# Optimization experiments

Hardware: AMD Instinct MI355X
Metric: run time of the kernel (lower is better)

Reference implementation:

```python
import jax, jax.numpy as jnp
import numpy as np

HIDDEN = 4096
N_HEADS = 32
N_KV_HEADS = 8
HEAD_DIM = HIDDEN // N_HEADS  # 128
GROUPS = N_HEADS // N_KV_HEADS  # 4
ATTN_MULT = 0.08838834764831845  # 1/sqrt(head_dim)
MAX_ATTN_VAL = 30.0
NEG_INF = -1e30


def setup_inputs() -> dict:
    key = jax.random.key(0)
    ks = jax.random.split(key, 5)
    B, S = 2, 2048
    hidden_states = jax.random.normal(ks[0], (B, S, HIDDEN), dtype=jnp.float32)
    scale = 1.0 / np.sqrt(HIDDEN)
    Wq = jax.random.normal(ks[1], (HIDDEN, N_HEADS * HEAD_DIM), dtype=jnp.float32) * scale
    Wk = jax.random.normal(ks[2], (HIDDEN, N_KV_HEADS * HEAD_DIM), dtype=jnp.float32) * scale
    Wv = jax.random.normal(ks[3], (HIDDEN, N_KV_HEADS * HEAD_DIM), dtype=jnp.float32) * scale
    Wo = jax.random.normal(ks[4], (N_HEADS * HEAD_DIM, HIDDEN), dtype=jnp.float32) * scale
    return {"hidden_states": hidden_states, "Wq": Wq, "Wk": Wk, "Wv": Wv, "Wo": Wo}


def reference(hidden_states, Wq, Wk, Wv, Wo):
    B, S, _ = hidden_states.shape
    # projections
    q = (hidden_states @ Wq).reshape(B, S, N_HEADS, HEAD_DIM).transpose(0, 2, 1, 3)      # bhsd
    k = (hidden_states @ Wk).reshape(B, S, N_KV_HEADS, HEAD_DIM).transpose(0, 2, 1, 3)   # bksd
    v = (hidden_states @ Wv).reshape(B, S, N_KV_HEADS, HEAD_DIM).transpose(0, 2, 1, 3)
    # GQA: expand kv heads to query heads
    k = jnp.repeat(k, GROUPS, axis=1)  # [B, N_HEADS, S, D]
    v = jnp.repeat(v, GROUPS, axis=1)
    # scaled scores with Grok-style tanh soft-cap
    scores = jnp.einsum('bhqd,bhkd->bhqk', q, k) * ATTN_MULT
    scores = MAX_ATTN_VAL * jnp.tanh(scores / MAX_ATTN_VAL)
    # causal mask
    causal = jnp.tril(jnp.ones((S, S), dtype=bool))
    scores = jnp.where(causal[None, None], scores, NEG_INF)
    probs = jax.nn.softmax(scores.astype(jnp.float32), axis=-1).astype(v.dtype)
    out = jnp.einsum('bhqk,bhkd->bhqd', probs, v)          # [B, H, S, D]
    out = out.transpose(0, 2, 1, 3).reshape(B, S, N_HEADS * HEAD_DIM)
    return out @ Wo
```

## Files before the change

### kernel.cpp

```cpp
#include <hip/hip_runtime.h>
#include <hip/hip_bf16.h>
#include <type_traits>
#include <cmath>

#define HIDDEN 4096
#define NHEADS 32
#define NKV 8
#define HD 128
#define BB 2
#define SS 2048
#define NTOK (BB*SS)
#define ATTN_MULT 0.08838834764831845f

using bf16x8 = __attribute__((ext_vector_type(8))) short;
using f32x4  = __attribute__((ext_vector_type(4))) float;

using gas = __attribute__((address_space(1))) const void;
using las = __attribute__((address_space(3))) void;

__device__ __forceinline__ unsigned short f2bf(float f){
  unsigned int u = __builtin_bit_cast(unsigned int, f);
  u += 0x7fffu + ((u >> 16) & 1u);
  return (unsigned short)(u >> 16);
}
__device__ __forceinline__ unsigned int cvtpk(float lo, float hi){
  unsigned int r;
  asm("v_cvt_pk_bf16_f32 %0, %1, %2" : "=v"(r) : "v"(lo), "v"(hi));
  return r;
}

__global__ void cvt_f32_bf16_k(const float* __restrict__ in, unsigned short* __restrict__ out, int n8){
  int i = blockIdx.x * blockDim.x + threadIdx.x;
  if (i >= n8) return;
  const float4* p = (const float4*)in + (size_t)i * 2;
  float4 a = p[0], b = p[1];
  bf16x8 o;
  o[0]=f2bf(a.x); o[1]=f2bf(a.y); o[2]=f2bf(a.z); o[3]=f2bf(a.w);
  o[4]=f2bf(b.x); o[5]=f2bf(b.y); o[6]=f2bf(b.z); o[7]=f2bf(b.w);
  ((bf16x8*)out)[i] = o;
}

__global__ void transpose_cvt_k(const float* __restrict__ W, unsigned short* __restrict__ WT, int K, int N){
  __shared__ float tile[32][33];
  int n0 = blockIdx.x * 32, k0 = blockIdx.y * 32;
  int tx = threadIdx.x, ty = threadIdx.y;
  #pragma unroll
  for (int i = 0; i < 4; ++i)
    tile[ty*4+i][tx] = W[(size_t)(k0 + ty*4 + i) * N + n0 + tx];
  __syncthreads();
  #pragma unroll
  for (int i = 0; i < 4; ++i)
    WT[(size_t)(n0 + ty*4 + i) * K + k0 + tx] = f2bf(tile[tx][ty*4+i]);
}

__global__ void transpose_v_k(const unsigned short* __restrict__ in, unsigned short* __restrict__ out){
  __shared__ unsigned short tile[32][33];
  int c0 = blockIdx.x * 32, r0 = blockIdx.y * 32;
  int tx = threadIdx.x, ty = threadIdx.y;
  #pragma unroll
  for (int i = 0; i < 4; ++i)
    tile[ty*4+i][tx] = in[(size_t)(r0 + ty*4 + i) * 2048 + 1024 + c0 + tx];
  __syncthreads();
  #pragma unroll
  for (int i = 0; i < 4; ++i){
    int c = c0 + ty*4 + i, r = r0 + tx;
    out[((size_t)((r >> 11) * 1024 + c)) * 2048 + (r & 2047)] = tile[tx][ty*4+i];
  }
}

template<typename OutT>
__global__ __launch_bounds__(256, 3)
void gemm_bt_k(const unsigned short* __restrict__ A,
               const unsigned short* __restrict__ BT,
               OutT* __restrict__ C, int M, int N, int K){
  __shared__ __align__(16) unsigned short As[128*32];
  __shared__ __align__(16) unsigned short Bs[128*32];
  const int m0 = blockIdx.y * 128, n0 = blockIdx.x * 128;
  const int tid = threadIdx.x, w = tid >> 6, lane = tid & 63;
  const int wr = w >> 1, wc = w & 1;
  const int lrow = lane & 15, lk = (lane >> 4) * 8;
  const int arow = lane >> 2, acol = (lane & 3) * 8;

  f32x4 acc[4][4] = {};

  for (int k0 = 0; k0 < K; k0 += 32){
    #pragma unroll
    for (int i = 0; i < 2; ++i){
      int chunk = w*2 + i;
      const unsigned short* ga = A  + (size_t)(m0 + chunk*16 + arow) * K + k0 + acol;
      const unsigned short* gb = BT + (size_t)(n0 + chunk*16 + arow) * K + k0 + acol;
      __builtin_amdgcn_global_load_lds((gas*)ga, (las*)(As + chunk*512), 16, 0, 0);
      __builtin_amdgcn_global_load_lds((gas*)gb, (las*)(Bs + chunk*512), 16, 0, 0);
    }
    __syncthreads();
    bf16x8 af[4], bfr[4];
    #pragma unroll
    for (int m = 0; m < 4; ++m) af[m]  = *(const bf16x8*)&As[(wr*64 + m*16 + lrow)*32 + lk];
    #pragma unroll
    for (int n = 0; n < 4; ++n) bfr[n] = *(const bf16x8*)&Bs[(wc*64 + n*16 + lrow)*32 + lk];
    #pragma unroll
    for (int m = 0; m < 4; ++m)
      #pragma unroll
      for (int n = 0; n < 4; ++n)
        acc[m][n] = __builtin_amdgcn_mfma_f32_16x16x32_bf16(af[m], bfr[n], acc[m][n], 0, 0, 0);
    __syncthreads();
  }

  const int crow = (lane >> 4) * 4, ccol = lane & 15;
  #pragma unroll
  for (int m = 0; m < 4; ++m)
    #pragma unroll
    for (int n = 0; n < 4; ++n){
      size_t base = (size_t)(m0 + wr*64 + m*16 + crow) * N + n0 + wc*64 + n*16 + ccol;
      #pragma unroll
      for (int r = 0; r < 4; ++r){
        float v = acc[m][n][r];
        if constexpr (std::is_same<OutT, unsigned short>::value) C[base + (size_t)r*N] = f2bf(v);
        else                                                     C[base + (size_t)r*N] = v;
      }
    }
}

#define GBAR() asm volatile("s_barrier" ::: "memory")

#define GEMM_PHASE(P, VMN, STAGE_STMT)                                          \
  {                                                                             \
    bf16x8 af[2][2];                                                            \
    _Pragma("unroll") for (int mi = 0; mi < 2; ++mi)                            \
    _Pragma("unroll") for (int kk = 0; kk < 2; ++kk){                           \
      int row = wm*128 + (P)*32 + mi*16 + lrow;                                 \
      int c8 = (kk*4 + lhi) ^ (row & 7);                                        \
      af[mi][kk] = *(const bf16x8*)&As[cur][row*64 + c8*8];                     \
    }                                                                           \
    if ((P) == 0){                                                              \
      _Pragma("unroll") for (int nf = 0; nf < 4; ++nf)                          \
      _Pragma("unroll") for (int kk = 0; kk < 2; ++kk){                         \
        int row = wn*64 + nf*16 + lrow;                                         \
        int c8 = (kk*4 + lhi) ^ (row & 7);                                      \
        bf[nf][kk] = *(const bf16x8*)&Bs[cur][row*64 + c8*8];                   \
      }                                                                         \
    }                                                                           \
    STAGE_STMT;                                                                 \
    asm volatile("s_waitcnt vmcnt(" #VMN ")");                                  \
    GBAR();                                                                     \
    __builtin_amdgcn_s_setprio(1);                                              \
    _Pragma("unroll") for (int mi = 0; mi < 2; ++mi)                            \
    _Pragma("unroll") for (int nf = 0; nf < 4; ++nf)                            \
    _Pragma("unroll") for (int kk = 0; kk < 2; ++kk)                            \
      acc[(P)*2+mi][nf] = __builtin_amdgcn_mfma_f32_16x16x32_bf16(              \
          af[mi][kk], bf[nf][kk], acc[(P)*2+mi][nf], 0, 0, 0);                  \
    __builtin_amdgcn_s_setprio(0);                                              \
    GBAR();                                                                     \
  }

template<typename OutT>
__global__ __launch_bounds__(512, 2)
void gemm8_k(const unsigned short* __restrict__ A,
             const unsigned short* __restrict__ BT,
             OutT* __restrict__ C, int M, int N, int K){
  __shared__ __align__(16) unsigned short As[2][256*64];
  __shared__ __align__(16) unsigned short Bs[2][256*64];

  const int nbx = N >> 8;
  const int id = blockIdx.x + blockIdx.y * nbx;
  const int nwg = nbx * (M >> 8);
  const int swz = (id & 7) * (nwg >> 3) + (id >> 3);
  const int m0 = (swz / nbx) << 8, n0 = (swz % nbx) << 8;

  const int tid = threadIdx.x, w = tid >> 6, lane = tid & 63;
  const int wm = w >> 2, wn = w & 3;
  const int lrow = lane & 15, lhi = lane >> 4;
  const int l3 = lane >> 3, k8l = lane & 7;
  const int NT = K >> 6;

  f32x4 acc[8][4] = {};
  bf16x8 bf[4][2];

  auto stageB = [&](int t, int s, int half){
    #pragma unroll
    for (int j = 0; j < 2; ++j){
      int row0 = half*128 + j*64 + w*8;
      int row = row0 + l3;
      const unsigned short* g = BT + (size_t)(n0 + row) * K + t*64 + ((k8l ^ (row & 7)) << 3);
      __builtin_amdgcn_global_load_lds((gas*)g, (las*)(&Bs[s][0] + row0*64), 16, 0, 0);
    }
  };
  auto stageA = [&](int t, int s, int g2){
    #pragma unroll
    for (int j = 0; j < 2; ++j){
      int g = g2 + j;
      int row0 = ((w >= 4) ? 128 : 0) + g*32 + (w & 3)*8;
      int row = row0 + l3;
      const unsigned short* ga = A + (size_t)(m0 + row) * K + t*64 + ((k8l ^ (row & 7)) << 3);
      __builtin_amdgcn_global_load_lds((gas*)ga, (las*)(&As[s][0] + row0*64), 16, 0, 0);
    }
  };

  stageB(0, 0, 0); stageB(0, 0, 1); stageA(0, 0, 0); stageA(0, 0, 2);
  asm volatile("s_waitcnt vmcnt(3)");
  GBAR();

  for (int t = 0; t < NT - 1; ++t){
    const int cur = t & 1, nxt = cur ^ 1;
    GEMM_PHASE(0, 4, stageB(t+1, nxt, 0));
    GEMM_PHASE(1, 5, stageB(t+1, nxt, 1));
    GEMM_PHASE(2, 6, stageA(t+1, nxt, 0));
    GEMM_PHASE(3, 3, stageA(t+1, nxt, 2));
  }
  {
    const int cur = (NT - 1) & 1;
    GEMM_PHASE(0, 2, (void)0);
    GEMM_PHASE(1, 1, (void)0);
    GEMM_PHASE(2, 0, (void)0);
    GEMM_PHASE(3, 0, (void)0);
  }

  #pragma unroll
  for (int mf = 0; mf < 8; ++mf)
    #pragma unroll
    for (int nf = 0; nf < 4; ++nf){
      size_t base = (size_t)(m0 + wm*128 + mf*16 + lhi*4) * N + n0 + wn*64 + nf*16 + lrow;
      #pragma unroll
      for (int r = 0; r < 4; ++r){
        float v = acc[mf][nf][r];
        if constexpr (std::is_same<OutT, unsigned short>::value) C[base + (size_t)r*N] = f2bf(v);
        else                                                     C[base + (size_t)r*N] = v;
      }
    }
}

__global__ __launch_bounds__(512, 2)
void attn_k(const unsigned short* __restrict__ Q,
            const unsigned short* __restrict__ KVp,
            const unsigned short* __restrict__ VTp,
            unsigned short* __restrict__ ctx){
  __shared__ __align__(16) unsigned short Ks[2][64*128];
  __shared__ __align__(16) unsigned short Vt[2][128*64];
  __shared__ __align__(16) unsigned short Ps[8][2048];

  const int Wb = blockIdx.x;
  const int xcd = Wb & 7, sI = Wb >> 3;
  const int idx = sI & 31, half = sI >> 5;
  const int a = idx & 3;
  const int qt = half ? a : 7 - a;
  const int hs = (idx >> 2) & 3, gsub = (idx >> 4) & 1;
  const int group = xcd*2 + gsub;
  const int b = group >> 3, kvh = group & 7;
  const int h = kvh*4 + hs;

  const int tid = threadIdx.x, w = tid >> 6, lane = tid & 63;
  const int q0 = qt * 256;
  const int nt = 4*qt + 4;
  const int lrow = lane & 15, lhi = lane >> 4;
  const int qwb = q0 + w*32;
  const int xorv = (lrow & 7) << 4;

  bf16x8 qf[2][4];
  {
    const unsigned short* qb = Q + (size_t)(b*SS + qwb + lrow) * 4096 + h*HD + lhi*8;
    #pragma unroll
    for (int qg = 0; qg < 2; ++qg)
      #pragma unroll
      for (int ks = 0; ks < 4; ++ks)
        qf[qg][ks] = *(const bf16x8*)(qb + (size_t)qg*16*4096 + ks*32);
  }

  f32x4 o[8][2] = {};
  float psum[2] = {0.f, 0.f};

  const unsigned short* Kbh  = KVp + (size_t)b * SS * 2048 + kvh * HD;
  const unsigned short* VTbh = VTp + ((size_t)b * 1024 + kvh * HD) * SS;

  auto STAGE = [&](int db, int t){
    #pragma unroll
    for (int it = 0; it < 2; ++it){
      int cbase = it*512 + w*64;
      int c = cbase + lane;
      int kkv = c >> 4, kc = c & 15;
      const unsigned short* gk = Kbh + (size_t)(t*64 + kkv) * 2048 + ((kc ^ (kkv & 7)) << 3);
      __builtin_amdgcn_global_load_lds((gas*)gk, (las*)(&Ks[db][0] + cbase*8), 16, 0, 0);
      int vd = c >> 3, vc = c & 7;
      const unsigned short* gv = VTbh + (size_t)vd * SS + t*64 + ((vc ^ ((vd ^ (vd >> 3)) & 7)) << 3);
      __builtin_amdgcn_global_load_lds((gas*)gv, (las*)(&Vt[db][0] + cbase*8), 16, 0, 0);
    }
  };

  STAGE(0, 0);
  __syncthreads();

  for (int t = 0; t < nt; ++t){
    const int db = t & 1;
    if (t + 1 < nt) STAGE(db ^ 1, t + 1);

    if (t*64 <= qwb + 31){
      const char* Kc = (const char*)&Ks[db][0];
      const char* Vc = (const char*)&Vt[db][0];
      char* Pw = (char*)&Ps[w][0];

      f32x4 sacc[2][4];
      #pragma unroll
      for (int cf = 0; cf < 4; ++cf){
        const int row = cf*16 + lrow;
        bf16x8 kf[4];
        #pragma unroll
        for (int ks = 0; ks < 4; ++ks){
          int kbyte = (row*256 + (ks*32 + lhi*8)*2) ^ ((row & 7) << 4);
          kf[ks] = *(const bf16x8*)(Kc + kbyte);
        }
        f32x4 s0 = {0.f,0.f,0.f,0.f}, s1 = {0.f,0.f,0.f,0.f};
        #pragma unroll
        for (int ks = 0; ks < 4; ++ks){
          s0 = __builtin_amdgcn_mfma_f32_16x16x32_bf16(kf[ks], qf[0][ks], s0, 0, 0, 0);
          s1 = __builtin_amdgcn_mfma_f32_16x16x32_bf16(kf[ks], qf[1][ks], s1, 0, 0, 0);
        }
        sacc[0][cf] = s0; sacc[1][cf] = s1;
      }

      #pragma unroll
      for (int qg = 0; qg < 2; ++qg){
        const int qglob = qwb + qg*16 + lrow;
        #pragma unroll
        for (int cf = 0; cf < 4; ++cf){
          float pv[4];
          #pragma unroll
          for (int r = 0; r < 4; ++r){
            float s = sacc[qg][cf][r] * ATTN_MULT;
            s = fminf(fmaxf(s, -25.f), 25.f);
            float s2 = s*s;
            float wv = __builtin_fmaf(s2, -3.7037037e-4f, 1.f);
            wv = __builtin_fmaf(s2*s2, 1.6460905e-7f, wv);
            float tt = s * wv;
            int kvg = t*64 + cf*16 + lhi*4 + r;
            float p = (kvg <= qglob) ? __expf(tt - 30.f) : 0.f;
            psum[qg] += p;
            pv[r] = p;
          }
          uint2 pk;
          pk.x = cvtpk(pv[0], pv[1]);
          pk.y = cvtpk(pv[2], pv[3]);
          *(uint2*)(Pw + qg*2048 + lrow*128 + ((cf*32 + lhi*8) ^ xorv)) = pk;
        }
      }

      #pragma unroll
      for (int hh = 0; hh < 2; ++hh){
        bf16x8 pf0 = *(const bf16x8*)(Pw +        lrow*128 + ((hh*64 + lhi*16) ^ xorv));
        bf16x8 pf1 = *(const bf16x8*)(Pw + 2048 + lrow*128 + ((hh*64 + lhi*16) ^ xorv));
        #pragma unroll
        for (int df = 0; df < 8; ++df){
          int d = df*16 + lrow;
          int vbyte = (d*128 + (hh*32 + lhi*8)*2) ^ (((d ^ (d >> 3)) & 7) << 4);
          bf16x8 vf = *(const bf16x8*)(Vc + vbyte);
          o[df][0] = __builtin_amdgcn_mfma_f32_16x16x32_bf16(vf, pf0, o[df][0], 0, 0, 0);
          o[df][1] = __builtin_amdgcn_mfma_f32_16x16x32_bf16(vf, pf1, o[df][1], 0, 0, 0);
        }
      }
    }
    __syncthreads();
  }

  #pragma unroll
  for (int qg = 0; qg < 2; ++qg){
    float sum = psum[qg];
    sum += __shfl_xor(sum, 16);
    sum += __shfl_xor(sum, 32);
    float inv = 1.f / sum;
    unsigned short* base = ctx + (size_t)(b*SS + qwb + qg*16 + lrow) * 4096 + h*HD + lhi*4;
    #pragma unroll
    for (int df = 0; df < 8; ++df){
      uint2 pk;
      pk.x = cvtpk(o[df][qg][0] * inv, o[df][qg][1] * inv);
      pk.y = cvtpk(o[df][qg][2] * inv, o[df][qg][3] * inv);
      *(uint2*)(base + df*16) = pk;
    }
  }
}

#define O_HSB   ((size_t)0)
#define O_WQT   ((size_t)33554432)
#define O_WKT   ((size_t)67108864)
#define O_WVT   ((size_t)75497472)
#define O_WOT   ((size_t)83886080)
#define O_Q     ((size_t)117440512)
#define O_KV    ((size_t)150994944)
#define O_CTX   ((size_t)167772160)
#define WS_NEED ((size_t)201326592)

extern "C" void kernel_launch(void* const* d_in, const int* in_sizes, int n_in,
                              void* d_out, int out_size, void* d_ws, size_t ws_size,
                              hipStream_t stream){
  if (ws_size < WS_NEED) return;
  const float* hs = (const float*)d_in[0];
  const float* Wq = (const float*)d_in[1];
  const float* Wk = (const float*)d_in[2];
  const float* Wv = (const float*)d_in[3];
  const float* Wo = (const float*)d_in[4];
  char* ws = (char*)d_ws;
  unsigned short* hsb = (unsigned short*)(ws + O_HSB);
  unsigned short* WqT = (unsigned short*)(ws + O_WQT);
  unsigned short* WkT = (unsigned short*)(ws + O_WKT);
  unsigned short* WvT = (unsigned short*)(ws + O_WVT);
  unsigned short* WoT = (unsigned short*)(ws + O_WOT);
  unsigned short* Qb  = (unsigned short*)(ws + O_Q);
  unsigned short* KVb = (unsigned short*)(ws + O_KV);
  unsigned short* ctxb= (unsigned short*)(ws + O_CTX);
  unsigned short* VTb = (unsigned short*)(ws + O_WQT);

  cvt_f32_bf16_k<<<dim3((NTOK*HIDDEN/8)/256), dim3(256), 0, stream>>>(hs, hsb, NTOK*HIDDEN/8);
  transpose_cvt_k<<<dim3(128,128), dim3(32,8), 0, stream>>>(Wq, WqT, 4096, 4096);
  transpose_cvt_k<<<dim3(32,128),  dim3(32,8), 0, stream>>>(Wk, WkT, 4096, 1024);
  transpose_cvt_k<<<dim3(32,128),  dim3(32,8), 0, stream>>>(Wv, WvT, 4096, 1024);
  transpose_cvt_k<<<dim3(128,128), dim3(32,8), 0, stream>>>(Wo, WoT, 4096, 4096);
  gemm8_k<unsigned short><<<dim3(16,16), dim3(512), 0, stream>>>(hsb, WqT, Qb, 4096, 4096, 4096);
  gemm_bt_k<unsigned short><<<dim3(16,32), dim3(256), 0, stream>>>(hsb, WkT, KVb, 4096, 2048, 4096);
  transpose_v_k<<<dim3(32,128), dim3(32,8), 0, stream>>>(KVb, VTb);
  attn_k<<<dim3(512), dim3(512), 0, stream>>>(Qb, KVb, VTb, ctxb);
  gemm8_k<float><<<dim3(16,16), dim3(512), 0, stream>>>(ctxb, WoT, (float*)d_out, 4096, 4096, 4096);
}
```

Measured before the change: 570.3 us.

## Fold attention scale into Q GEMM, use gemm8 for KV, streamline softmax path

The KV projection now uses the larger pipelined gemm8 kernel instead of the simple 128x128 GEMM. The attention multiplier is folded into the Q projection epilogue, and the soft-cap/exp is rewritten with base-2 constants, fmed3 clamping and raw v_exp_f32. Causal masking runs only on the diagonal tile via a templated lambda. The P scratch buffer is halved by interleaving P generation with PV MFMAs per half-tile, launch bounds are raised to 4 blocks per CU, and setprio wraps the MFMA bursts. Rounding Q to bf16 after scaling shifts precision slightly, and the raised occupancy target may force register spills.

```diff
diff --git a/kernel.cpp b/kernel.cpp
--- a/kernel.cpp
+++ b/kernel.cpp
@@ -1,6 +1,7 @@
 #include <hip/hip_runtime.h>
 #include <hip/hip_bf16.h>
 #include <type_traits>
+#include <utility>
 #include <cmath>
 
 #define HIDDEN 4096
@@ -28,6 +29,16 @@
   asm("v_cvt_pk_bf16_f32 %0, %1, %2" : "=v"(r) : "v"(lo), "v"(hi));
   return r;
 }
+__device__ __forceinline__ float exp2_hw(float x){
+  float r;
+  asm("v_exp_f32 %0, %1" : "=v"(r) : "v"(x));
+  return r;
+}
+
+#define LOG2E 1.4426950408889634f
+#define C1L  (-5.3433149e-4f)
+#define C2L  (2.3748069e-7f)
+#define B30L (-43.280851227f)
 
 __global__ void cvt_f32_bf16_k(const float* __restrict__ in, unsigned short* __restrict__ out, int n8){
   int i = blockIdx.x * blockDim.x + threadIdx.x;
@@ -66,59 +77,6 @@
     int c = c0 + ty*4 + i, r = r0 + tx;
     out[((size_t)((r >> 11) * 1024 + c)) * 2048 + (r & 2047)] = tile[tx][ty*4+i];
   }
-}
-
-template<typename OutT>
-__global__ __launch_bounds__(256, 3)
-void gemm_bt_k(const unsigned short* __restrict__ A,
-               const unsigned short* __restrict__ BT,
-               OutT* __restrict__ C, int M, int N, int K){
-  __shared__ __align__(16) unsigned short As[128*32];
-  __shared__ __align__(16) unsigned short Bs[128*32];
-  const int m0 = blockIdx.y * 128, n0 = blockIdx.x * 128;
-  const int tid = threadIdx.x, w = tid >> 6, lane = tid & 63;
-  const int wr = w >> 1, wc = w & 1;
-  const int lrow = lane & 15, lk = (lane >> 4) * 8;
-  const int arow = lane >> 2, acol = (lane & 3) * 8;
-
-  f32x4 acc[4][4] = {};
-
-  for (int k0 = 0; k0 < K; k0 += 32){
-    #pragma unroll
-    for (int i = 0; i < 2; ++i){
-      int chunk = w*2 + i;
-      const unsigned short* ga = A  + (size_t)(m0 + chunk*16 + arow) * K + k0 + acol;
-      const unsigned short* gb = BT + (size_t)(n0 + chunk*16 + arow) * K + k0 + acol;
-      __builtin_amdgcn_global_load_lds((gas*)ga, (las*)(As + chunk*512), 16, 0, 0);
-      __builtin_amdgcn_global_load_lds((gas*)gb, (las*)(Bs + chunk*512), 16, 0, 0);
-    }
-    __syncthreads();
-    bf16x8 af[4], bfr[4];
-    #pragma unroll
-    for (int m = 0; m < 4; ++m) af[m]  = *(const bf16x8*)&As[(wr*64 + m*16 + lrow)*32 + lk];
-    #pragma unroll
-    for (int n = 0; n < 4; ++n) bfr[n] = *(const bf16x8*)&Bs[(wc*64 + n*16 + lrow)*32 + lk];
-    #pragma unroll
-    for (int m = 0; m < 4; ++m)
-      #pragma unroll
-      for (int n = 0; n < 4; ++n)
-        acc[m][n] = __builtin_amdgcn_mfma_f32_16x16x32_bf16(af[m], bfr[n], acc[m][n], 0, 0, 0);
-    __syncthreads();
-  }
-
-  const int crow = (lane >> 4) * 4, ccol = lane & 15;
-  #pragma unroll
-  for (int m = 0; m < 4; ++m)
-    #pragma unroll
-    for (int n = 0; n < 4; ++n){
-      size_t base = (size_t)(m0 + wr*64 + m*16 + crow) * N + n0 + wc*64 + n*16 + ccol;
-      #pragma unroll
-      for (int r = 0; r < 4; ++r){
-        float v = acc[m][n][r];
-        if constexpr (std::is_same<OutT, unsigned short>::value) C[base + (size_t)r*N] = f2bf(v);
-        else                                                     C[base + (size_t)r*N] = v;
-      }
-    }
 }
 
 #define GBAR() asm volatile("s_barrier" ::: "memory")
@@ -157,7 +115,7 @@
 __global__ __launch_bounds__(512, 2)
 void gemm8_k(const unsigned short* __restrict__ A,
              const unsigned short* __restrict__ BT,
-             OutT* __restrict__ C, int M, int N, int K){
+             OutT* __restrict__ C, int M, int N, int K, float scale){
   __shared__ __align__(16) unsigned short As[2][256*64];
   __shared__ __align__(16) unsigned short Bs[2][256*64];
 
@@ -222,38 +180,38 @@
       size_t base = (size_t)(m0 + wm*128 + mf*16 + lhi*4) * N + n0 + wn*64 + nf*16 + lrow;
       #pragma unroll
       for (int r = 0; r < 4; ++r){
-        float v = acc[mf][nf][r];
+        float v = acc[mf][nf][r] * scale;
         if constexpr (std::is_same<OutT, unsigned short>::value) C[base + (size_t)r*N] = f2bf(v);
         else                                                     C[base + (size_t)r*N] = v;
       }
     }
 }
 
-__global__ __launch_bounds__(512, 2)
+__global__ __launch_bounds__(512, 4)
 void attn_k(const unsigned short* __restrict__ Q,
             const unsigned short* __restrict__ KVp,
             const unsigned short* __restrict__ VTp,
             unsigned short* __restrict__ ctx){
   __shared__ __align__(16) unsigned short Ks[2][64*128];
   __shared__ __align__(16) unsigned short Vt[2][128*64];
-  __shared__ __align__(16) unsigned short Ps[8][2048];
+  __shared__ __align__(16) unsigned short Ps[8][1024];
 
   const int Wb = blockIdx.x;
   const int xcd = Wb & 7, sI = Wb >> 3;
-  const int idx = sI & 31, half = sI >> 5;
-  const int a = idx & 3;
-  const int qt = half ? a : 7 - a;
-  const int hs = (idx >> 2) & 3, gsub = (idx >> 4) & 1;
+  const int pair = sI >> 1, po = sI & 1;
+  const int a = pair & 3;
+  const int qt = po ? a : 7 - a;
+  const int hsH = (pair >> 2) & 3, gsub = (pair >> 4) & 1;
   const int group = xcd*2 + gsub;
   const int b = group >> 3, kvh = group & 7;
-  const int h = kvh*4 + hs;
+  const int h = kvh*4 + hsH;
 
   const int tid = threadIdx.x, w = tid >> 6, lane = tid & 63;
   const int q0 = qt * 256;
   const int nt = 4*qt + 4;
   const int lrow = lane & 15, lhi = lane >> 4;
   const int qwb = q0 + w*32;
-  const int xorv = (lrow & 7) << 4;
+  const int xorv = (lrow & 3) << 4;
 
   bf16x8 qf[2][4];
   {
@@ -308,53 +266,62 @@
           kf[ks] = *(const bf16x8*)(Kc + kbyte);
         }
         f32x4 s0 = {0.f,0.f,0.f,0.f}, s1 = {0.f,0.f,0.f,0.f};
+        __builtin_amdgcn_s_setprio(1);
         #pragma unroll
         for (int ks = 0; ks < 4; ++ks){
           s0 = __builtin_amdgcn_mfma_f32_16x16x32_bf16(kf[ks], qf[0][ks], s0, 0, 0, 0);
           s1 = __builtin_amdgcn_mfma_f32_16x16x32_bf16(kf[ks], qf[1][ks], s1, 0, 0, 0);
         }
+        __builtin_amdgcn_s_setprio(0);
         sacc[0][cf] = s0; sacc[1][cf] = s1;
       }
 
-      #pragma unroll
-      for (int qg = 0; qg < 2; ++qg){
-        const int qglob = qwb + qg*16 + lrow;
+      auto body = [&](auto DIAG){
         #pragma unroll
-        for (int cf = 0; cf < 4; ++cf){
-          float pv[4];
+        for (int hh = 0; hh < 2; ++hh){
           #pragma unroll
-          for (int r = 0; r < 4; ++r){
-            float s = sacc[qg][cf][r] * ATTN_MULT;
-            s = fminf(fmaxf(s, -25.f), 25.f);
-            float s2 = s*s;
-            float wv = __builtin_fmaf(s2, -3.7037037e-4f, 1.f);
-            wv = __builtin_fmaf(s2*s2, 1.6460905e-7f, wv);
-            float tt = s * wv;
-            int kvg = t*64 + cf*16 + lhi*4 + r;
-            float p = (kvg <= qglob) ? __expf(tt - 30.f) : 0.f;
-            psum[qg] += p;
-            pv[r] = p;
+          for (int qg = 0; qg < 2; ++qg){
+            const int qglob = qwb + qg*16 + lrow;
+            #pragma unroll
+            for (int cc = 0; cc < 2; ++cc){
+              const int cf = hh*2 + cc;
+              float pv[4];
+              #pragma unroll
+              for (int r = 0; r < 4; ++r){
+                float s = __builtin_amdgcn_fmed3f(sacc[qg][cf][r], -25.f, 25.f);
+                float s2 = s*s, s4 = s2*s2;
+                float wv = __builtin_fmaf(s2, C1L, LOG2E);
+                wv = __builtin_fmaf(s4, C2L, wv);
+                float p = exp2_hw(__builtin_fmaf(s, wv, B30L));
+                if constexpr (decltype(DIAG)::value){
+                  int kvg = t*64 + cf*16 + lhi*4 + r;
+                  p = (kvg <= qglob) ? p : 0.f;
+                }
+                psum[qg] += p;
+                pv[r] = p;
+              }
+              uint2 pk;
+              pk.x = cvtpk(pv[0], pv[1]);
+              pk.y = cvtpk(pv[2], pv[3]);
+              *(uint2*)(Pw + qg*1024 + lrow*64 + ((cc*32 + lhi*8) ^ xorv)) = pk;
+            }
           }
-          uint2 pk;
-          pk.x = cvtpk(pv[0], pv[1]);
-          pk.y = cvtpk(pv[2], pv[3]);
-          *(uint2*)(Pw + qg*2048 + lrow*128 + ((cf*32 + lhi*8) ^ xorv)) = pk;
+          bf16x8 pf0 = *(const bf16x8*)(Pw +        lrow*64 + ((lhi*16) ^ xorv));
+          bf16x8 pf1 = *(const bf16x8*)(Pw + 1024 + lrow*64 + ((lhi*16) ^ xorv));
+          __builtin_amdgcn_s_setprio(1);
+          #pragma unroll
+          for (int df = 0; df < 8; ++df){
+            int d = df*16 + lrow;
+            int vbyte = (d*128 + (hh*32 + lhi*8)*2) ^ (((d ^ (d >> 3)) & 7) << 4);
+            bf16x8 vf = *(const bf16x8*)(Vc + vbyte);
+            o[df][0] = __builtin_amdgcn_mfma_f32_16x16x32_bf16(vf, pf0, o[df][0], 0, 0, 0);
+            o[df][1] = __builtin_amdgcn_mfma_f32_16x16x32_bf16(vf, pf1, o[df][1], 0, 0, 0);
+          }
+          __builtin_amdgcn_s_setprio(0);
         }
-      }
-
-      #pragma unroll
-      for (int hh = 0; hh < 2; ++hh){
-        bf16x8 pf0 = *(const bf16x8*)(Pw +        lrow*128 + ((hh*64 + lhi*16) ^ xorv));
-        bf16x8 pf1 = *(const bf16x8*)(Pw + 2048 + lrow*128 + ((hh*64 + lhi*16) ^ xorv));
-        #pragma unroll
-        for (int df = 0; df < 8; ++df){
-          int d = df*16 + lrow;
-          int vbyte = (d*128 + (hh*32 + lhi*8)*2) ^ (((d ^ (d >> 3)) & 7) << 4);
-          bf16x8 vf = *(const bf16x8*)(Vc + vbyte);
-          o[df][0] = __builtin_amdgcn_mfma_f32_16x16x32_bf16(vf, pf0, o[df][0], 0, 0, 0);
-          o[df][1] = __builtin_amdgcn_mfma_f32_16x16x32_bf16(vf, pf1, o[df][1], 0, 0, 0);
-        }
-      }
+      };
+      if (t == (qwb >> 6)) body(std::true_type{});
+      else                 body(std::false_type{});
     }
     __syncthreads();
   }
@@ -411,9 +378,9 @@
   transpose_cvt_k<<<dim3(32,128),  dim3(32,8), 0, stream>>>(Wk, WkT, 4096, 1024);
   transpose_cvt_k<<<dim3(32,128),  dim3(32,8), 0, stream>>>(Wv, WvT, 4096, 1024);
   transpose_cvt_k<<<dim3(128,128), dim3(32,8), 0, stream>>>(Wo, WoT, 4096, 4096);
-  gemm8_k<unsigned short><<<dim3(16,16), dim3(512), 0, stream>>>(hsb, WqT, Qb, 4096, 4096, 4096);
-  gemm_bt_k<unsigned short><<<dim3(16,32), dim3(256), 0, stream>>>(hsb, WkT, KVb, 4096, 2048, 4096);
+  gemm8_k<unsigned short><<<dim3(16,16), dim3(512), 0, stream>>>(hsb, WqT, Qb, 4096, 4096, 4096, ATTN_MULT);
+  gemm8_k<unsigned short><<<dim3(8,16),  dim3(512), 0, stream>>>(hsb, WkT, KVb, 4096, 2048, 4096, 1.0f);
   transpose_v_k<<<dim3(32,128), dim3(32,8), 0, stream>>>(KVb, VTb);
   attn_k<<<dim3(512), dim3(512), 0, stream>>>(Qb, KVb, VTb, ctxb);
-  gemm8_k<float><<<dim3(16,16), dim3(512), 0, stream>>>(ctxb, WoT, (float*)d_out, 4096, 4096, 4096);
-}
+  gemm8_k<float><<<dim3(16,16), dim3(512), 0, stream>>>(ctxb, WoT, (float*)d_out, 4096, 4096, 4096, 1.0f);
+}
```

Measured after the change: 1.059 ms. +85.7%, slower.
